# Optimization experiments

Measured on AMD Instinct MI355X. Metric: run time of the kernel, lower is better.

## Reference

```python
import jax, jax.numpy as jnp
import numpy as np

NUM_SEG = 16
FRAMES_PER_SEG = 25
T = NUM_SEG * FRAMES_PER_SEG  # 400
PROPOSALS = jnp.array([(s, e) for s in range(NUM_SEG) for e in range(s, NUM_SEG)], dtype=jnp.int32)  # [136,2]
B, L, DV, DS, D = 16, 32, 4096, 768, 1024


def setup_inputs() -> dict:
    key = jax.random.key(0)
    ks = jax.random.split(key, 5)
    videos = jax.random.normal(ks[0], (B, T, DV), dtype=jnp.float32)
    sentences = jax.random.normal(ks[1], (B, L, DS), dtype=jnp.float32)
    Wv = jax.random.normal(ks[2], (DV, D), dtype=jnp.float32) * 0.02
    bv = jnp.zeros((D,), dtype=jnp.float32)
    Ws = jax.random.normal(ks[3], (DS, D), dtype=jnp.float32) * 0.02
    bs = jnp.zeros((D,), dtype=jnp.float32)
    idx = jax.random.randint(ks[4], (B,), 0, PROPOSALS.shape[0])
    y_true = PROPOSALS[idx]  # each ground-truth matches exactly one proposal
    return {"videos": videos, "sentences": sentences, "Wv": Wv, "bv": bv,
            "Ws": Ws, "bs": bs, "y_true": y_true}


def reference(videos, sentences, Wv, bv, Ws, bs, y_true):
    # sub-model representations (stand-ins for video_layer / sentence_layer)
    Vr = videos @ Wv + bv          # [B,T,D]
    Sr = sentences @ Ws + bs       # [B,L,D]
    # keras Attention: scores = Q @ K^T (K=V=video window), softmax over keys, out = attn @ V
    scores = jnp.einsum('bld,btd->blt', Sr, Vr)  # [B,L,T] computed once, masked per proposal
    t = jnp.arange(T)
    starts = PROPOSALS[:, 0] * FRAMES_PER_SEG
    ends = (PROPOSALS[:, 1] + 1) * FRAMES_PER_SEG
    mask = (t[None, :] >= starts[:, None]) & (t[None, :] < ends[:, None])  # [P,T]
    masked = jnp.where(mask[None, :, None, :], scores[:, None, :, :], -jnp.inf)  # [B,P,L,T]
    attn = jax.nn.softmax(masked, axis=-1)
    out = jnp.einsum('bplt,btd->bpld', attn, Vr)  # [B,P,L,D] weighted context per proposal
    # cosine_similarity along axis=0 (the L axis) -> one score vector of length D per proposal
    num = jnp.sum(out * Sr[:, None, :, :], axis=2)                     # [B,P,D]
    den = jnp.linalg.norm(out, axis=2) * jnp.linalg.norm(Sr, axis=1)[:, None, :]
    score = num / (den + 1e-15)                                        # [B,P,D]
    match = jnp.all(PROPOSALS[None, :, :] == y_true[:, None, :], axis=-1)  # [B,P]
    positive = jnp.sum(jnp.where(match[..., None], score, 0.0), axis=1)    # [B,D]
    negative = jnp.max(jnp.where(match[..., None], -jnp.inf, score), axis=(1, 2))  # [B] (tf.reduce_max over all)
    return positive, negative
```

## Files before the change

kernel.cpp:

```cpp
#include <hip/hip_runtime.h>

typedef _Float16 f16;
typedef f16 f16x4 __attribute__((ext_vector_type(4)));
typedef f16 f16x8 __attribute__((ext_vector_type(8)));
typedef float f32x4 __attribute__((ext_vector_type(4)));

__global__ void k_cast(const float* __restrict__ src, f16* __restrict__ dst, int n4) {
    int i = blockIdx.x * 256 + threadIdx.x;
    if (i < n4) {
        f32x4 v = *(const f32x4*)(src + (size_t)i * 4);
        f16x4 h = { (f16)v[0], (f16)v[1], (f16)v[2], (f16)v[3] };
        *(f16x4*)(dst + (size_t)i * 4) = h;
    }
}

__global__ __launch_bounds__(256) void k_transpose_cast(const float* __restrict__ src,
                                                        f16* __restrict__ dst, int R, int C) {
    __shared__ float tile[32 * 33];
    int tx = threadIdx.x & 31, ty = threadIdx.x >> 5;
    int c0 = blockIdx.x * 32, r0 = blockIdx.y * 32;
#pragma unroll
    for (int i = 0; i < 4; ++i) {
        int r = ty + i * 8;
        tile[r * 33 + tx] = src[(size_t)(r0 + r) * C + c0 + tx];
    }
    __syncthreads();
#pragma unroll
    for (int i = 0; i < 4; ++i) {
        int rr = ty + i * 8;
        dst[(size_t)(c0 + rr) * R + r0 + tx] = (f16)tile[tx * 33 + rr];
    }
}

__global__ __launch_bounds__(512, 2) void k_gemm2(const f16* __restrict__ A, const f16* __restrict__ Bt,
                                                  const float* __restrict__ bias, f16* __restrict__ Ch) {
    constexpr int K = 4096, N = 1024;
    constexpr int BUF = 49152;
    __shared__ __attribute__((aligned(16))) char smem[3 * BUF];
    const int tid = threadIdx.x;
    const int lane = tid & 63, wave = tid >> 6;
    const int wm = wave >> 2, wn = wave & 3;
    const int lr = lane & 15, lq = lane >> 4;
    const int orig = blockIdx.x;
    const int wg = (orig & 7) * 25 + (orig >> 3);
    const int mt = wg >> 3, nt = wg & 7;
    const int m0 = mt * 256, n0 = nt * 128;
    const int srow = tid >> 3;
    const int scol = ((tid & 7) ^ ((tid >> 3) & 7)) * 8;
    const f16* aA = A + (size_t)(m0 + srow) * K + scol;
    const f16* aB = Bt + (size_t)(n0 + srow) * K + scol;
    constexpr int NT = K / 64;

    auto stage = [&](int bb, int kt) {
        const f16* a0 = aA + kt * 64;
        const f16* b0 = aB + kt * 64;
        char* la = smem + bb + tid * 16;
#pragma unroll
        for (int i = 0; i < 4; ++i)
            __builtin_amdgcn_global_load_lds(
                (const __attribute__((address_space(1))) void*)(a0 + (size_t)i * 64 * K),
                (__attribute__((address_space(3))) void*)(la + i * 8192), 16, 0, 0);
        char* lb = smem + bb + 32768 + tid * 16;
#pragma unroll
        for (int i = 0; i < 2; ++i)
            __builtin_amdgcn_global_load_lds(
                (const __attribute__((address_space(1))) void*)(b0 + (size_t)i * 64 * K),
                (__attribute__((address_space(3))) void*)(lb + i * 8192), 16, 0, 0);
    };

    f32x4 acc[8][2] = {};
    const int xa = (lr & 7) << 4;

    stage(0, 0);
    stage(BUF, 1);
    stage(2 * BUF, 2);
    asm volatile("s_waitcnt vmcnt(12)" ::: "memory");
    __builtin_amdgcn_s_barrier();

    int bb = 0;
    for (int t = 0; t < NT; ++t) {
        const char* Ab = smem + bb;
        const char* Bb = smem + bb + 32768;
#pragma unroll
        for (int ks = 0; ks < 2; ++ks) {
            const int co = (ks * 64 + lq * 16) ^ xa;
            f16x8 bf0 = *(const f16x8*)(Bb + (wn * 32 + lr) * 128 + co);
            f16x8 bf1 = *(const f16x8*)(Bb + (wn * 32 + 16 + lr) * 128 + co);
            __builtin_amdgcn_s_setprio(1);
#pragma unroll
            for (int m = 0; m < 8; ++m) {
                f16x8 af = *(const f16x8*)(Ab + (wm * 128 + m * 16 + lr) * 128 + co);
                acc[m][0] = __builtin_amdgcn_mfma_f32_16x16x32_f16(af, bf0, acc[m][0], 0, 0, 0);
                acc[m][1] = __builtin_amdgcn_mfma_f32_16x16x32_f16(af, bf1, acc[m][1], 0, 0, 0);
            }
            __builtin_amdgcn_s_setprio(0);
        }
        __builtin_amdgcn_s_barrier();
        if (t + 3 < NT) {
            stage(bb, t + 3);
            asm volatile("s_waitcnt vmcnt(12)" ::: "memory");
        } else if (t + 2 < NT) {
            asm volatile("s_waitcnt vmcnt(6)" ::: "memory");
        } else if (t + 1 < NT) {
            asm volatile("s_waitcnt vmcnt(0)" ::: "memory");
        }
        if (t + 1 < NT) {
            __builtin_amdgcn_s_barrier();
            __builtin_amdgcn_sched_barrier(0);
        }
        bb = (bb == 2 * BUF) ? 0 : bb + BUF;
    }

#pragma unroll
    for (int m = 0; m < 8; ++m) {
#pragma unroll
        for (int n = 0; n < 2; ++n) {
            int col = n0 + wn * 32 + n * 16 + lr;
            float bc = bias[col];
#pragma unroll
            for (int j = 0; j < 4; ++j) {
                int row = m0 + wm * 128 + m * 16 + lq * 4 + j;
                Ch[(size_t)row * N + col] = (f16)(acc[m][n][j] + bc);
            }
        }
    }
}

__global__ __launch_bounds__(256) void k_gemm(const f16* __restrict__ A, const f16* __restrict__ Bt,
                                              const float* __restrict__ bias, float* __restrict__ C,
                                              f16* __restrict__ Ch, int M, int N, int K) {
    __shared__ f16 As[128 * 64];
    __shared__ f16 Bs[128 * 64];
    const int tid = threadIdx.x;
    const int lane = tid & 63, wave = tid >> 6;
    const int wr = wave >> 1, wc = wave & 1;
    const int m0 = blockIdx.y * 128, n0 = blockIdx.x * 128;
    const int lr = lane & 15, lq = lane >> 4;
    f32x4 acc[4][4] = {};
    for (int k0 = 0; k0 < K; k0 += 64) {
        __syncthreads();
#pragma unroll
        for (int r = 0; r < 4; ++r) {
            int o = r * 4096 + tid * 16;
            int row = o >> 7;
            int kb = (o & 127) >> 1;
            __builtin_amdgcn_global_load_lds(
                (const __attribute__((address_space(1))) void*)(A + (size_t)(m0 + row) * K + k0 + kb),
                (__attribute__((address_space(3))) void*)((char*)As + o), 16, 0, 0);
        }
#pragma unroll
        for (int r = 0; r < 4; ++r) {
            int o = r * 4096 + tid * 16;
            int row = o >> 7;
            int kb = (o & 127) >> 1;
            __builtin_amdgcn_global_load_lds(
                (const __attribute__((address_space(1))) void*)(Bt + (size_t)(n0 + row) * K + k0 + kb),
                (__attribute__((address_space(3))) void*)((char*)Bs + o), 16, 0, 0);
        }
        __syncthreads();
#pragma unroll
        for (int ks = 0; ks < 2; ++ks) {
            f16x8 af[4], bf[4];
#pragma unroll
            for (int m = 0; m < 4; ++m)
                af[m] = *(const f16x8*)&As[(wr * 64 + m * 16 + lr) * 64 + ks * 32 + lq * 8];
#pragma unroll
            for (int n = 0; n < 4; ++n)
                bf[n] = *(const f16x8*)&Bs[(wc * 64 + n * 16 + lr) * 64 + ks * 32 + lq * 8];
#pragma unroll
            for (int m = 0; m < 4; ++m)
#pragma unroll
                for (int n = 0; n < 4; ++n)
                    acc[m][n] = __builtin_amdgcn_mfma_f32_16x16x32_f16(af[m], bf[n], acc[m][n], 0, 0, 0);
        }
    }
#pragma unroll
    for (int m = 0; m < 4; ++m) {
#pragma unroll
        for (int n = 0; n < 4; ++n) {
            int col = n0 + wc * 64 + n * 16 + lr;
            float bcol = bias[col];
#pragma unroll
            for (int j = 0; j < 4; ++j) {
                int row = m0 + wr * 64 + m * 16 + lq * 4 + j;
                float v = acc[m][n][j] + bcol;
                C[(size_t)row * N + col] = v;
                Ch[(size_t)row * N + col] = (f16)v;
            }
        }
    }
}

__global__ void k_srnorm(const float* __restrict__ Sr, float* __restrict__ SrNorm) {
    int idx = blockIdx.x * 256 + threadIdx.x;
    int b = idx >> 10, d = idx & 1023;
    float s = 0.f;
#pragma unroll
    for (int l = 0; l < 32; ++l) {
        float v = Sr[((size_t)(b * 32 + l)) * 1024 + d];
        s += v * v;
    }
    SrNorm[idx] = sqrtf(s);
}

__global__ __launch_bounds__(256) void k_seg(const f16* __restrict__ Vrh, const f16* __restrict__ Srh,
                                             float* __restrict__ W, float* __restrict__ Mg,
                                             float* __restrict__ Eg) {
    const int b = blockIdx.x >> 4, k = blockIdx.x & 15;
    __shared__ float Sm[32 * 26];
    __shared__ float P[32 * 25];
    __shared__ float VrB[25 * 260];
    const int tid = threadIdx.x;
    const int lane = tid & 63, wave = tid >> 6;
    {
        const int mf = wave >> 1, nf = wave & 1;
        const int lr = lane & 15, lq = lane >> 4;
        f32x4 acc = {};
        const f16* arow = Srh + ((size_t)(b * 32 + mf * 16 + lr)) * 1024 + lq * 8;
        const f16* brow = Vrh + ((size_t)(b * 400 + k * 25 + nf * 16 + lr)) * 1024 + lq * 8;
        for (int k0 = 0; k0 < 1024; k0 += 32) {
            f16x8 a = *(const f16x8*)(arow + k0);
            f16x8 bb = *(const f16x8*)(brow + k0);
            acc = __builtin_amdgcn_mfma_f32_16x16x32_f16(a, bb, acc, 0, 0, 0);
        }
        int t = nf * 16 + lr;
        if (t < 25) {
#pragma unroll
            for (int j = 0; j < 4; ++j) {
                int l = mf * 16 + lq * 4 + j;
                Sm[l * 26 + t] = acc[j];
            }
        }
    }
    __syncthreads();
    if (tid < 32) {
        int l = tid;
        float m = Sm[l * 26];
        for (int t = 1; t < 25; ++t) m = fmaxf(m, Sm[l * 26 + t]);
        float e = 0.f;
        for (int t = 0; t < 25; ++t) {
            float p = __expf(Sm[l * 26 + t] - m);
            P[l * 25 + t] = p;
            e += p;
        }
        Mg[(b * 16 + k) * 32 + l] = m;
        Eg[(b * 16 + k) * 32 + l] = e;
    }
    __syncthreads();
    const int dl = tid & 63, q = tid >> 6;
    for (int c = 0; c < 4; ++c) {
#pragma unroll
        for (int ii = 0; ii < 7; ++ii) {
            int idx4 = tid + ii * 256;
            if (idx4 < 1600) {
                int row = idx4 >> 6, d4 = (idx4 & 63) * 4;
                f16x4 h = *(const f16x4*)&Vrh[((size_t)(b * 400 + k * 25 + row)) * 1024 + c * 256 + d4];
                f32x4 f = { (float)h[0], (float)h[1], (float)h[2], (float)h[3] };
                *(f32x4*)&VrB[row * 260 + d4] = f;
            }
        }
        __syncthreads();
        f32x4 accw[8] = {};
        for (int t = 0; t < 25; ++t) {
            f32x4 v = *(const f32x4*)&VrB[t * 260 + dl * 4];
#pragma unroll
            for (int li = 0; li < 8; ++li) {
                float p = P[(q + li * 4) * 25 + t];
                accw[li][0] += p * v[0];
                accw[li][1] += p * v[1];
                accw[li][2] += p * v[2];
                accw[li][3] += p * v[3];
            }
        }
#pragma unroll
        for (int li = 0; li < 8; ++li) {
            int l = q + li * 4;
            *(f32x4*)&W[(((size_t)(b * 32 + l)) * 16 + k) * 1024 + c * 256 + dl * 4] = accw[li];
        }
        __syncthreads();
    }
}

__global__ __launch_bounds__(512) void k_alpha(const float* __restrict__ Mg, const float* __restrict__ Eg,
                                               float* __restrict__ EMg, float* __restrict__ rdeng) {
    const int b = blockIdx.x;
    __shared__ float EE[32 * 16];
    __shared__ int pS[136], pE[136];
    const int tid = threadIdx.x;
    if (tid < 136) {
        int s = 0, rem = tid;
        while (rem >= 16 - s) { rem -= 16 - s; ++s; }
        pS[tid] = s;
        pE[tid] = s + rem;
    }
    if (tid < 32) {
        int l = tid;
        float G = -1e30f;
#pragma unroll
        for (int k = 0; k < 16; ++k) G = fmaxf(G, Mg[(b * 16 + k) * 32 + l]);
#pragma unroll
        for (int k = 0; k < 16; ++k) {
            float em = __expf(Mg[(b * 16 + k) * 32 + l] - G);
            EMg[((size_t)(b * 32 + l)) * 16 + k] = em;
            EE[l * 16 + k] = em * Eg[(b * 16 + k) * 32 + l];
        }
    }
    __syncthreads();
    for (int it = tid; it < 136 * 32; it += 512) {
        int p = it >> 5, l = it & 31;
        float den = 0.f;
        int s = pS[p], e = pE[p];
        for (int k = s; k <= e; ++k) den += EE[l * 16 + k];
        rdeng[((size_t)(b * 136) + p) * 32 + l] = 1.0f / (den + 1e-30f);
    }
}

__global__ __launch_bounds__(512) void k_combine(const float* __restrict__ W, const float* __restrict__ EMg,
                                                 const float* __restrict__ rdeng, const float* __restrict__ Sr,
                                                 const float* __restrict__ SrNorm, const int* __restrict__ ytrue,
                                                 float* __restrict__ out, unsigned int* __restrict__ negk) {
    extern __shared__ float v_s[];
    __shared__ float wmax_s[8];
    const int b = blockIdx.x >> 4, dc = blockIdx.x & 15;
    const int tid = threadIdx.x, lane = tid & 63, wave = tid >> 6;
    const int d = dc * 64 + lane;

#pragma unroll 4
    for (int i = 0; i < 64; ++i) {
        int idx = tid + i * 512;
        int l = idx >> 10, k = (idx >> 6) & 15;
        float em = EMg[(b * 32 + l) * 16 + k];
        v_s[idx] = W[(((size_t)(b * 32 + l)) * 16 + k) * 1024 + dc * 64 + (idx & 63)] * em;
    }
    float sr[32];
#pragma unroll
    for (int l = 0; l < 32; ++l) sr[l] = Sr[((size_t)(b * 32 + l)) * 1024 + d];
    const float srn = SrNorm[b * 1024 + d];
    const int sy = ytrue[b * 2], ey = ytrue[b * 2 + 1];
    const int pm = sy * 16 - (sy * (sy - 1)) / 2 + (ey - sy);
    __syncthreads();

    const int sA = wave, sB = 15 - wave;
    const int pA0 = sA * 16 - (sA * (sA - 1)) / 2 - sA;
    const int pB0 = sB * 16 - (sB * (sB - 1)) / 2 - sB;
    float runA[32], runB[32];
#pragma unroll
    for (int l = 0; l < 32; ++l) { runA[l] = 0.f; runB[l] = 0.f; }
    float lmax = -1e30f;

    for (int e = sA; e < 16; ++e) {
        const bool doB = (e >= sB);
        const int pA = pA0 + e, pB = pB0 + e;
        f32x4 rdA[8], rdB[8];
        const float* rA = rdeng + ((size_t)b * 136 + pA) * 32;
        const float* rB = rdeng + ((size_t)b * 136 + pB) * 32;
#pragma unroll
        for (int j = 0; j < 8; ++j) rdA[j] = *(const f32x4*)(rA + j * 4);
        if (doB) {
#pragma unroll
            for (int j = 0; j < 8; ++j) rdB[j] = *(const f32x4*)(rB + j * 4);
        }
        float numA = 0.f, ssqA = 0.f, numB = 0.f, ssqB = 0.f;
#pragma unroll
        for (int l = 0; l < 32; ++l) {
            float ve = v_s[(l * 16 + e) * 64 + lane];
            runA[l] += ve;
            float t = runA[l] * rdA[l >> 2][l & 3];
            numA += t * sr[l];
            ssqA += t * t;
            if (doB) {
                runB[l] += ve;
                float tb = runB[l] * rdB[l >> 2][l & 3];
                numB += tb * sr[l];
                ssqB += tb * tb;
            }
        }
        float scoreA = numA / (sqrtf(ssqA) * srn + 1e-15f);
        if (pA == pm) out[b * 1024 + d] = scoreA;
        else lmax = fmaxf(lmax, scoreA);
        if (doB) {
            float scoreB = numB / (sqrtf(ssqB) * srn + 1e-15f);
            if (pB == pm) out[b * 1024 + d] = scoreB;
            else lmax = fmaxf(lmax, scoreB);
        }
    }
#pragma unroll
    for (int off = 32; off >= 1; off >>= 1) lmax = fmaxf(lmax, __shfl_xor(lmax, off));
    if (lane == 0) wmax_s[wave] = lmax;
    __syncthreads();
    if (tid == 0) {
        float m = wmax_s[0];
#pragma unroll
        for (int w = 1; w < 8; ++w) m = fmaxf(m, wmax_s[w]);
        unsigned u = __float_as_uint(m);
        unsigned key = (u & 0x80000000u) ? ~u : (u | 0x80000000u);
        atomicMax(&negk[b], key);
    }
}

__global__ void k_init(unsigned* __restrict__ negk) {
    if (threadIdx.x < 16) negk[threadIdx.x] = 0u;
}

__global__ void k_negout(const unsigned* __restrict__ negk, float* __restrict__ out) {
    int i = threadIdx.x;
    if (i < 16) {
        unsigned key = negk[i];
        unsigned u = (key & 0x80000000u) ? (key ^ 0x80000000u) : ~key;
        out[16384 + i] = __uint_as_float(u);
    }
}

extern "C" void kernel_launch(void* const* d_in, const int* in_sizes, int n_in,
                              void* d_out, int out_size, void* d_ws, size_t ws_size,
                              hipStream_t stream) {
    const float* videos = (const float*)d_in[0];
    const float* sentences = (const float*)d_in[1];
    const float* Wv = (const float*)d_in[2];
    const float* bv = (const float*)d_in[3];
    const float* Ws = (const float*)d_in[4];
    const float* bs = (const float*)d_in[5];
    const int* ytrue = (const int*)d_in[6];
    float* out = (float*)d_out;

    char* ws = (char*)d_ws;
    size_t off = 0;
    auto alloc = [&](size_t bytes) {
        char* p = ws + off;
        off = (off + bytes + 255) & ~(size_t)255;
        return p;
    };
    f16* vh = (f16*)alloc(52428800);
    f16* wvt = (f16*)alloc(8388608);
    f16* sh = (f16*)alloc(786432);
    f16* wst = (f16*)alloc(1572864);
    f16* Vrh = (f16*)alloc(13107200);
    float* Sr = (float*)alloc(2097152);
    f16* Srh = (f16*)alloc(1048576);
    float* W = (float*)alloc(33554432);
    float* Mg = (float*)alloc(32768);
    float* Eg = (float*)alloc(32768);
    float* EMg = (float*)alloc(32768);
    float* rdeng = (float*)alloc(278528);
    float* SrNorm = (float*)alloc(65536);
    unsigned* negk = (unsigned*)alloc(64);
    if (off > ws_size) return;

    hipLaunchKernelGGL(k_init, dim3(1), dim3(64), 0, stream, negk);
    hipLaunchKernelGGL(k_cast, dim3(6553600 / 256), dim3(256), 0, stream, videos, vh, 6553600);
    hipLaunchKernelGGL(k_cast, dim3(98304 / 256), dim3(256), 0, stream, sentences, sh, 98304);
    hipLaunchKernelGGL(k_transpose_cast, dim3(32, 128), dim3(256), 0, stream, Wv, wvt, 4096, 1024);
    hipLaunchKernelGGL(k_transpose_cast, dim3(32, 24), dim3(256), 0, stream, Ws, wst, 768, 1024);
    hipLaunchKernelGGL(k_gemm2, dim3(200), dim3(512), 0, stream, vh, wvt, bv, Vrh);
    hipLaunchKernelGGL(k_gemm, dim3(8, 4), dim3(256), 0, stream, sh, wst, bs, Sr, Srh, 512, 1024, 768);
    hipLaunchKernelGGL(k_srnorm, dim3(64), dim3(256), 0, stream, Sr, SrNorm);
    hipLaunchKernelGGL(k_seg, dim3(256), dim3(256), 0, stream, Vrh, Srh, W, Mg, Eg);
    hipLaunchKernelGGL(k_alpha, dim3(16), dim3(512), 0, stream, Mg, Eg, EMg, rdeng);
    hipLaunchKernelGGL(k_combine, dim3(256), dim3(512), 131072, stream, W, EMg, rdeng, Sr, SrNorm, ytrue, out, negk);
    hipLaunchKernelGGL(k_negout, dim3(1), dim3(64), 0, stream, negk, out);
}
```

Baseline: 333.7 us.

## Merge cast and transpose launches, store segment context W in fp16

```diff
diff --git a/kernel.cpp b/kernel.cpp
--- a/kernel.cpp
+++ b/kernel.cpp
@@ -5,20 +5,38 @@
 typedef f16 f16x8 __attribute__((ext_vector_type(8)));
 typedef float f32x4 __attribute__((ext_vector_type(4)));
 
-__global__ void k_cast(const float* __restrict__ src, f16* __restrict__ dst, int n4) {
+__global__ void k_cast2(const float* __restrict__ srcA, f16* __restrict__ dstA, int nA,
+                        const float* __restrict__ srcB, f16* __restrict__ dstB, int nB) {
     int i = blockIdx.x * 256 + threadIdx.x;
-    if (i < n4) {
-        f32x4 v = *(const f32x4*)(src + (size_t)i * 4);
-        f16x4 h = { (f16)v[0], (f16)v[1], (f16)v[2], (f16)v[3] };
-        *(f16x4*)(dst + (size_t)i * 4) = h;
-    }
-}
-
-__global__ __launch_bounds__(256) void k_transpose_cast(const float* __restrict__ src,
-                                                        f16* __restrict__ dst, int R, int C) {
+    const float* s;
+    f16* d;
+    if (i < nA) {
+        s = srcA + (size_t)i * 4;
+        d = dstA + (size_t)i * 4;
+    } else if (i < nA + nB) {
+        int j = i - nA;
+        s = srcB + (size_t)j * 4;
+        d = dstB + (size_t)j * 4;
+    } else {
+        return;
+    }
+    f32x4 v = *(const f32x4*)s;
+    f16x4 h = { (f16)v[0], (f16)v[1], (f16)v[2], (f16)v[3] };
+    *(f16x4*)d = h;
+}
+
+__global__ __launch_bounds__(256) void k_tc2(const float* __restrict__ Wv, f16* __restrict__ wvt,
+                                             const float* __restrict__ Ws, f16* __restrict__ wst) {
     __shared__ float tile[32 * 33];
+    const int C = 1024;
+    int y = blockIdx.y;
+    const float* src;
+    f16* dst;
+    int R, r0;
+    if (y < 128) { src = Wv; dst = wvt; R = 4096; r0 = y * 32; }
+    else { src = Ws; dst = wst; R = 768; r0 = (y - 128) * 32; }
     int tx = threadIdx.x & 31, ty = threadIdx.x >> 5;
-    int c0 = blockIdx.x * 32, r0 = blockIdx.y * 32;
+    int c0 = blockIdx.x * 32;
 #pragma unroll
     for (int i = 0; i < 4; ++i) {
         int r = ty + i * 8;
@@ -204,7 +222,7 @@
 }
 
 __global__ __launch_bounds__(256) void k_seg(const f16* __restrict__ Vrh, const f16* __restrict__ Srh,
-                                             float* __restrict__ W, float* __restrict__ Mg,
+                                             f16* __restrict__ W, float* __restrict__ Mg,
                                              float* __restrict__ Eg) {
     const int b = blockIdx.x >> 4, k = blockIdx.x & 15;
     __shared__ float Sm[32 * 26];
@@ -275,18 +293,21 @@
 #pragma unroll
         for (int li = 0; li < 8; ++li) {
             int l = q + li * 4;
-            *(f32x4*)&W[(((size_t)(b * 32 + l)) * 16 + k) * 1024 + c * 256 + dl * 4] = accw[li];
+            f16x4 h = { (f16)accw[li][0], (f16)accw[li][1], (f16)accw[li][2], (f16)accw[li][3] };
+            *(f16x4*)&W[(((size_t)(b * 32 + l)) * 16 + k) * 1024 + c * 256 + dl * 4] = h;
         }
         __syncthreads();
     }
 }
 
 __global__ __launch_bounds__(512) void k_alpha(const float* __restrict__ Mg, const float* __restrict__ Eg,
-                                               float* __restrict__ EMg, float* __restrict__ rdeng) {
+                                               float* __restrict__ EMg, float* __restrict__ rdeng,
+                                               unsigned int* __restrict__ negk) {
     const int b = blockIdx.x;
     __shared__ float EE[32 * 16];
     __shared__ int pS[136], pE[136];
     const int tid = threadIdx.x;
+    if (tid == 0) negk[b] = 0u;
     if (tid < 136) {
         int s = 0, rem = tid;
         while (rem >= 16 - s) { rem -= 16 - s; ++s; }
@@ -315,7 +336,7 @@
     }
 }
 
-__global__ __launch_bounds__(512) void k_combine(const float* __restrict__ W, const float* __restrict__ EMg,
+__global__ __launch_bounds__(512) void k_combine(const f16* __restrict__ W, const float* __restrict__ EMg,
                                                  const float* __restrict__ rdeng, const float* __restrict__ Sr,
                                                  const float* __restrict__ SrNorm, const int* __restrict__ ytrue,
                                                  float* __restrict__ out, unsigned int* __restrict__ negk) {
@@ -330,7 +351,7 @@
         int idx = tid + i * 512;
         int l = idx >> 10, k = (idx >> 6) & 15;
         float em = EMg[(b * 32 + l) * 16 + k];
-        v_s[idx] = W[(((size_t)(b * 32 + l)) * 16 + k) * 1024 + dc * 64 + (idx & 63)] * em;
+        v_s[idx] = (float)W[(((size_t)(b * 32 + l)) * 16 + k) * 1024 + dc * 64 + (idx & 63)] * em;
     }
     float sr[32];
 #pragma unroll
@@ -396,10 +417,6 @@
         unsigned key = (u & 0x80000000u) ? ~u : (u | 0x80000000u);
         atomicMax(&negk[b], key);
     }
-}
-
-__global__ void k_init(unsigned* __restrict__ negk) {
-    if (threadIdx.x < 16) negk[threadIdx.x] = 0u;
 }
 
 __global__ void k_negout(const unsigned* __restrict__ negk, float* __restrict__ out) {
@@ -437,7 +454,7 @@
     f16* Vrh = (f16*)alloc(13107200);
     float* Sr = (float*)alloc(2097152);
     f16* Srh = (f16*)alloc(1048576);
-    float* W = (float*)alloc(33554432);
+    f16* W = (f16*)alloc(16777216);
     float* Mg = (float*)alloc(32768);
     float* Eg = (float*)alloc(32768);
     float* EMg = (float*)alloc(32768);
@@ -446,16 +463,14 @@
     unsigned* negk = (unsigned*)alloc(64);
     if (off > ws_size) return;
 
-    hipLaunchKernelGGL(k_init, dim3(1), dim3(64), 0, stream, negk);
-    hipLaunchKernelGGL(k_cast, dim3(6553600 / 256), dim3(256), 0, stream, videos, vh, 6553600);
-    hipLaunchKernelGGL(k_cast, dim3(98304 / 256), dim3(256), 0, stream, sentences, sh, 98304);
-    hipLaunchKernelGGL(k_transpose_cast, dim3(32, 128), dim3(256), 0, stream, Wv, wvt, 4096, 1024);
-    hipLaunchKernelGGL(k_transpose_cast, dim3(32, 24), dim3(256), 0, stream, Ws, wst, 768, 1024);
+    hipLaunchKernelGGL(k_cast2, dim3((6553600 + 98304 + 255) / 256), dim3(256), 0, stream,
+                       videos, vh, 6553600, sentences, sh, 98304);
+    hipLaunchKernelGGL(k_tc2, dim3(32, 152), dim3(256), 0, stream, Wv, wvt, Ws, wst);
     hipLaunchKernelGGL(k_gemm2, dim3(200), dim3(512), 0, stream, vh, wvt, bv, Vrh);
     hipLaunchKernelGGL(k_gemm, dim3(8, 4), dim3(256), 0, stream, sh, wst, bs, Sr, Srh, 512, 1024, 768);
     hipLaunchKernelGGL(k_srnorm, dim3(64), dim3(256), 0, stream, Sr, SrNorm);
     hipLaunchKernelGGL(k_seg, dim3(256), dim3(256), 0, stream, Vrh, Srh, W, Mg, Eg);
-    hipLaunchKernelGGL(k_alpha, dim3(16), dim3(512), 0, stream, Mg, Eg, EMg, rdeng);
+    hipLaunchKernelGGL(k_alpha, dim3(16), dim3(512), 0, stream, Mg, Eg, EMg, rdeng, negk);
     hipLaunchKernelGGL(k_combine, dim3(256), dim3(512), 131072, stream, W, EMg, rdeng, Sr, SrNorm, ytrue, out, negk);
     hipLaunchKernelGGL(k_negout, dim3(1), dim3(64), 0, stream, negk, out);
 }
```

Result: no change. 329.0 us (-1.4%).
